# Kernel tuning notes

Hardware: AMD Instinct MI355X
Metric: run time of the kernel (lower is better)

## Reference

```python
import math
import jax, jax.numpy as jnp
import numpy as np

B, N, D_MODEL, H = 2, 4096, 2048, 16
HEAD_DIM = D_MODEL // H
CHUNK = 128  # chunk length for the lightning-attention recurrence


def _slopes(n_heads):
    # ALiBi-style slopes used by lightning attention (n_heads is a power of 2)
    start = 2.0 ** (-(2.0 ** -(math.log2(n_heads) - 3)))
    return np.array([start ** (i + 1) for i in range(n_heads)], dtype=np.float32)


def setup_inputs() -> dict:
    key = jax.random.key(0)
    kx, k1, k2, k3, k4 = jax.random.split(key, 5)
    scale = 1.0 / math.sqrt(D_MODEL)
    x = jax.random.normal(kx, (B, N, D_MODEL), dtype=jnp.float32)
    w_qkv = jax.random.normal(k1, (3 * D_MODEL, D_MODEL), dtype=jnp.float32) * scale
    b_qkv = jax.random.normal(k2, (3 * D_MODEL,), dtype=jnp.float32) * 0.01
    w_out = jax.random.normal(k3, (D_MODEL, D_MODEL), dtype=jnp.float32) * scale
    b_out = jax.random.normal(k4, (D_MODEL,), dtype=jnp.float32) * 0.01
    return {"x": x, "w_qkv": w_qkv, "b_qkv": b_qkv, "w_out": w_out, "b_out": b_out}


def _lightning_attn(q, k, v):
    # q,k,v: (B, H, N, d). Causal linear attention with per-head decay lam:
    #   S_t = lam * S_{t-1} + k_t v_t^T ;  o_t = q_t S_t
    b, h, n, d = q.shape
    nc = n // CHUNK
    lam = jnp.exp(-jnp.asarray(_slopes(h)))  # (H,)

    pos = jnp.arange(CHUNK, dtype=jnp.float32)
    decay_q = lam[:, None] ** (pos + 1.0)            # (H, C) inter-chunk q scaling
    decay_k = lam[:, None] ** (CHUNK - 1.0 - pos)    # (H, C) state-update k scaling
    diff = pos[:, None] - pos[None, :]
    causal = diff >= 0
    dmask = jnp.where(causal, lam[:, None, None] ** jnp.maximum(diff, 0.0), 0.0)  # (H,C,C)
    lam_c = lam ** CHUNK                              # (H,)

    def to_chunks(t):
        return t.reshape(b, h, nc, CHUNK, d).transpose(2, 0, 1, 3, 4)  # (nc,B,H,C,d)

    qc, kc, vc = to_chunks(q), to_chunks(k), to_chunks(v)

    def step(S, inp):
        qb, kb, vb = inp  # each (B,H,C,d); S: (B,H,d,d)
        inter = jnp.einsum('bhcd,bhde->bhce', qb * decay_q[None, :, :, None], S)
        scores = jnp.einsum('bhcd,bhed->bhce', qb, kb) * dmask[None]
        intra = jnp.einsum('bhce,bhed->bhcd', scores, vb)
        S_new = lam_c[None, :, None, None] * S + jnp.einsum(
            'bhcd,bhce->bhde', kb * decay_k[None, :, :, None], vb)
        return S_new, inter + intra

    S0 = jnp.zeros((b, h, d, d), dtype=q.dtype)
    _, out = jax.lax.scan(step, S0, (qc, kc, vc))  # out: (nc,B,H,C,d)
    return out.transpose(1, 2, 0, 3, 4).reshape(b, h, n, d)


def reference(x, w_qkv, b_qkv, w_out, b_out):
    b, n, dm = x.shape
    qkv = x @ w_qkv.T + b_qkv                         # (B,N,3D)
    q, k, v = jnp.split(qkv, 3, axis=-1)
    def heads(t):
        return t.reshape(b, n, H, HEAD_DIM).transpose(0, 2, 1, 3)  # (B,H,N,d)
    attn = _lightning_attn(heads(q), heads(k), heads(v))
    attn = attn.transpose(0, 2, 1, 3).reshape(b, n, dm)
    return attn @ w_out.T + b_out
```

## Files before the change

kernel.cpp:

```cpp
#include <hip/hip_runtime.h>
#include <stdint.h>

#define DM    2048
#define NSEQ  4096
#define BB    2
#define NH    16
#define HD    128
#define CHK   128
#define NCHK  32
#define NBH   (BB*NH)
#define MTOT  (BB*NSEQ)
#define N3    (3*DM)

typedef unsigned short u16;
typedef unsigned int   u32;
typedef __attribute__((ext_vector_type(8))) short s16x8;
typedef __attribute__((ext_vector_type(4))) short s16x4;
typedef __attribute__((ext_vector_type(4))) float f32x4;
typedef __attribute__((ext_vector_type(2))) unsigned short u16x2;

__device__ __forceinline__ float b2f(u16 b){ u32 u = ((u32)b) << 16; float f; __builtin_memcpy(&f,&u,4); return f; }
__device__ __forceinline__ u16 f2b(float f){ u32 u; __builtin_memcpy(&u,&f,4); u += 0x7fffu + ((u>>16)&1u); return (u16)(u>>16); }

__device__ __forceinline__ void gload16(const u16* g, u16* l){
  __builtin_amdgcn_global_load_lds((const __attribute__((address_space(1))) void*)g,
                                   (__attribute__((address_space(3))) void*)l, 16, 0, 0);
}

__global__ __launch_bounds__(256) void conv_bf16(const float* __restrict__ src,
                                                 u16* __restrict__ dst, int n4)
{
  for (int i = blockIdx.x*blockDim.x + threadIdx.x; i < n4; i += gridDim.x*blockDim.x){
    f32x4 v = *(const f32x4*)(src + (size_t)i*4);
    s16x4 o;
    #pragma unroll
    for (int j=0;j<4;j++) o[j] = (short)f2b(v[j]);
    *(s16x4*)(dst + (size_t)i*4) = o;
  }
}


#define GEMM256_CORE(GA_, GB_)                                                  \
  __shared__ u16 lds[65536];                                       \
  const int tid  = threadIdx.x;                                                 \
  const int lane = tid & 63;                                                    \
  const int w    = tid >> 6;                                                    \
  const int wm_i = w >> 2, wn_i = w & 3;                                        \
  const int m0 = blockIdx.y << 8;                                               \
  const int n0 = blockIdx.x << 8;                                               \
  const int l15 = lane & 15, lg = lane >> 4, l7 = lane & 7;                     \
  const int c0 = ((lg)     ^ l7) << 3;                      \
  const int c1 = ((4 + lg) ^ l7) << 3;                      \
  const int abase = wm_i*8192 + l15*64;                                         \
  const int bbase = 32768 + (wn_i>>1)*8192 + (wn_i&1)*4096 + l15*64;            \
  const int grow = lane >> 3;                                                   \
  const int gcol = ((lane & 7) ^ grow) * 8;                                     \
  const u16* gAl = GA_ + (size_t)(m0 + grow)*DM + gcol;                         \
  const u16* gBl = GB_ + (size_t)(n0 + grow)*DM + gcol;                         \
  auto STG = [&](const u16* gl, int ldsbase, int h, int kt){                    \
    _Pragma("unroll")                                                           \
    for (int j=0;j<2;j++)                                                       \
      gload16(gl + ((size_t)(h*128 + j*64 + w*8))*DM + (size_t)kt*64,           \
              lds + ldsbase + (j*64 + w*8)*64);                                 \
  };                                                                            \
  f32x4 acc[8][4];                                                              \
  _Pragma("unroll")                                                             \
  for (int m=0;m<8;m++)                                                         \
    _Pragma("unroll")                                                           \
    for (int n=0;n<4;n++) acc[m][n] = f32x4{0.f,0.f,0.f,0.f};                   \
  s16x8 bfr[4][2];                                                              \
   \
  STG(gBl, 32768,             0, 0); STG(gBl, 32768+8192,       1, 0);          \
  STG(gAl, 0,                 0, 0); STG(gAl, 8192,             1, 0);          \
  STG(gBl, 32768+16384,       0, 1); STG(gBl, 32768+16384+8192, 1, 1);          \
  asm volatile("s_waitcnt vmcnt(4)" ::: "memory");                              \
  __builtin_amdgcn_s_barrier();                                                 \
  for (int it=0; it<15; ++it){                                                  \
    const int k1 = 2*it+1, k2 = 2*it+2, k3 = 2*it+3;                            \
    PH(0,0, STG(gAl, 16384,             0, k1), );                              \
    PH(0,1, STG(gAl, 16384+8192,        1, k1), );                              \
    PH(0,2, STG(gBl, 32768,             0, k2), );                              \
    PH(0,3, STG(gBl, 32768+8192,        1, k2),                                 \
            asm volatile("s_waitcnt vmcnt(4)" ::: "memory"));                   \
    PH(1,0, STG(gAl, 0,                 0, k2), );                              \
    PH(1,1, STG(gAl, 8192,              1, k2), );                              \
    PH(1,2, STG(gBl, 32768+16384,       0, k3), );                              \
    PH(1,3, STG(gBl, 32768+16384+8192,  1, k3),                                 \
            asm volatile("s_waitcnt vmcnt(4)" ::: "memory"));                   \
  }                                                                             \
                      \
  PH(0,0, STG(gAl, 16384,      0, 31), );                                       \
  PH(0,1, STG(gAl, 16384+8192, 1, 31), );                                       \
  PH(0,2, (void)0, );                                                           \
  PH(0,3, (void)0, asm volatile("s_waitcnt vmcnt(0)" ::: "memory"));            \
  PH(1,0, (void)0, ); PH(1,1, (void)0, );                                       \
  PH(1,2, (void)0, ); PH(1,3, (void)0, );

#define PH(D, Q, STAGE, VM) do{                                                 \
  s16x8 af[2][2];                                                               \
  if ((Q)==0){                                                                  \
    _Pragma("unroll")                                                           \
    for (int n=0;n<4;n++){                                                      \
      bfr[n][0] = *(const s16x8*)(lds + bbase + (D)*16384 + n*1024 + c0);       \
      bfr[n][1] = *(const s16x8*)(lds + bbase + (D)*16384 + n*1024 + c1);       \
    }                                                                           \
  }                                                                             \
  af[0][0] = *(const s16x8*)(lds + abase + (D)*16384 + (2*(Q)  )*1024 + c0);    \
  af[0][1] = *(const s16x8*)(lds + abase + (D)*16384 + (2*(Q)  )*1024 + c1);    \
  af[1][0] = *(const s16x8*)(lds + abase + (D)*16384 + (2*(Q)+1)*1024 + c0);    \
  af[1][1] = *(const s16x8*)(lds + abase + (D)*16384 + (2*(Q)+1)*1024 + c1);    \
  STAGE;                                                                        \
  VM;                                                                           \
  __builtin_amdgcn_s_barrier();                                                 \
  __builtin_amdgcn_s_setprio(1);                                                \
  _Pragma("unroll")                                                             \
  for (int kk=0;kk<2;kk++)                                                      \
    _Pragma("unroll")                                                           \
    for (int mm=0;mm<2;mm++)                                                    \
      _Pragma("unroll")                                                         \
      for (int n=0;n<4;n++)                                                     \
        acc[2*(Q)+mm][n] = __builtin_amdgcn_mfma_f32_16x16x32_bf16(             \
            af[mm][kk], bfr[n][kk], acc[2*(Q)+mm][n], 0,0,0);                   \
  __builtin_amdgcn_s_setprio(0);                                                \
}while(0)

__global__ __launch_bounds__(512, 2) void gemm_qkv(const u16* __restrict__ Xb,
    const u16* __restrict__ Wb, const float* __restrict__ bias,
    u16* __restrict__ Qb, u16* __restrict__ Kb, u16* __restrict__ Vb)
{
  GEMM256_CORE(Xb, Wb)

  #pragma unroll
  for (int n=0;n<4;n++){
    const int gn = n0 + wn_i*64 + n*16 + l15;
    const float bv = bias[gn];
    const int which = gn >> 11;
    const int h = (gn >> 7) & 15;
    const int e = gn & 127;
    u16* base_ = (which==0) ? Qb : ((which==1) ? Kb : Vb);
    #pragma unroll
    for (int m=0;m<8;m++){
      #pragma unroll
      for (int r=0;r<4;r++){
        const int gm = m0 + wm_i*128 + m*16 + lg*4 + r;
        const int b  = gm >> 12;
        const int tt = gm & (NSEQ-1);
        base_[(((size_t)(b*NH + h))*NSEQ + tt)*HD + e] = f2b(acc[m][n][r] + bv);
      }
    }
  }
}

__global__ __launch_bounds__(512, 2) void gemm_out(const u16* __restrict__ Ab,
    const u16* __restrict__ Wb, const float* __restrict__ bias,
    float* __restrict__ Out)
{
  GEMM256_CORE(Ab, Wb)

  #pragma unroll
  for (int n=0;n<4;n++){
    const int gn = n0 + wn_i*64 + n*16 + l15;
    const float bv = bias[gn];
    #pragma unroll
    for (int m=0;m<8;m++){
      #pragma unroll
      for (int r=0;r<4;r++){
        const int gm = m0 + wm_i*128 + m*16 + lg*4 + r;
        Out[(size_t)gm*DM + gn] = acc[m][n][r] + bv;
      }
    }
  }
}

__global__ __launch_bounds__(256) void chunk_kv(const u16* __restrict__ Kb,
    const u16* __restrict__ Vb, u16* __restrict__ USb)
{
  __shared__ short Kt[128][152];
  __shared__ short Vt[128][152];
  const int tid = threadIdx.x;
  const int blk = blockIdx.x;
  const int c  = blk & (NCHK-1);
  const int bh = blk >> 5;
  const int h  = bh & (NH-1);
  const float slope = exp2f(-0.5f*(float)(h+1));

  const u16* kg = Kb + ((size_t)bh*NSEQ + (size_t)c*CHK)*HD;
  const u16* vg = Vb + ((size_t)bh*NSEQ + (size_t)c*CHK)*HD;

  const int e0 = (tid & 63) * 2;
  const int tq = tid >> 6;
  #pragma unroll
  for (int it=0; it<4; it++){
    const int tb = it*32 + tq*8;
    s16x8 k0v, k1v, v0v, v1v;
    #pragma unroll
    for (int j=0;j<8;j++){
      const int t = tb + j;
      u16x2 kv = *(const u16x2*)(kg + (size_t)t*HD + e0);
      u16x2 vv = *(const u16x2*)(vg + (size_t)t*HD + e0);
      const float dk = expf(-slope*(float)(CHK-1-t));
      k0v[j] = (short)f2b(b2f(kv[0])*dk);
      k1v[j] = (short)f2b(b2f(kv[1])*dk);
      v0v[j] = (short)vv[0];
      v1v[j] = (short)vv[1];
    }
    *(s16x8*)&Kt[e0  ][tb] = k0v;
    *(s16x8*)&Kt[e0+1][tb] = k1v;
    *(s16x8*)&Vt[e0  ][tb] = v0v;
    *(s16x8*)&Vt[e0+1][tb] = v1v;
  }
  __syncthreads();

  const int lane = tid & 63;
  const int l15 = lane & 15, lg = lane >> 4;
  const int w = tid >> 6;
  const int wm = (w >> 1) << 6, wn = (w & 1) << 6;
  f32x4 acc[4][4];
  #pragma unroll
  for (int i=0;i<4;i++)
    #pragma unroll
    for (int j=0;j<4;j++) acc[i][j] = f32x4{0.f,0.f,0.f,0.f};

  #pragma unroll
  for (int ks=0; ks<4; ks++){
    const int kk = ks*32 + lg*8;
    s16x8 af[4], bf[4];
    #pragma unroll
    for (int m=0;m<4;m++) af[m] = *(const s16x8*)&Kt[wm + m*16 + l15][kk];
    #pragma unroll
    for (int n=0;n<4;n++) bf[n] = *(const s16x8*)&Vt[wn + n*16 + l15][kk];
    #pragma unroll
    for (int m=0;m<4;m++)
      #pragma unroll
      for (int n=0;n<4;n++)
        acc[m][n] = __builtin_amdgcn_mfma_f32_16x16x32_bf16(af[m], bf[n], acc[m][n], 0,0,0);
  }

  u16* up = USb + (size_t)blk*(HD*HD);
  #pragma unroll
  for (int m=0;m<4;m++)
    #pragma unroll
    for (int n=0;n<4;n++)
      #pragma unroll
      for (int r=0;r<4;r++){
        const int d = wm + m*16 + lg*4 + r;
        const int f = wn + n*16 + l15;
        up[d*HD + f] = f2b(acc[m][n][r]);
      }
}

__global__ __launch_bounds__(256) void scan_state(u16* __restrict__ USb)
{
  const int bh = blockIdx.x >> 3;
  const int rs = blockIdx.x & 7;
  const int tid = threadIdx.x;
  const int h = bh & (NH-1);
  const float slope = exp2f(-0.5f*(float)(h+1));
  const float lamC = expf(-slope*(float)CHK);
  float s[8];
  #pragma unroll
  for (int i=0;i<8;i++) s[i]=0.f;
  u16* base = USb + (size_t)bh*NCHK*HD*HD + rs*2048;
  const int off = tid*8;
  for (int c=0;c<NCHK;c++){
    u16* p = base + (size_t)c*HD*HD + off;
    s16x8 u = *(const s16x8*)p;
    s16x8 wv;
    #pragma unroll
    for (int j=0;j<8;j++) wv[j] = (short)f2b(s[j]);
    *(s16x8*)p = wv;
    #pragma unroll
    for (int j=0;j<8;j++) s[j] = lamC*s[j] + b2f((u16)u[j]);
  }
}

__global__ __launch_bounds__(512) void attn_chunk(
    const u16* __restrict__ Qb, const u16* __restrict__ Kb, const u16* __restrict__ Vb,
    const u16* __restrict__ Sb, u16* __restrict__ ATT)
{
  __shared__ short alds[73728];
  short* Qs = alds;
  short* Ks = alds + 17408;
  short* Vt = alds + 34816;
  short* St = alds + 54272;

  const int tid = threadIdx.x;
  const int blk = blockIdx.x;
  const int c  = blk & (NCHK-1);
  const int bh = blk >> 5;
  const int b  = bh >> 4, h = bh & 15;
  const float slope = exp2f(-0.5f*(float)(h+1));

  const size_t qoff = ((size_t)bh*NSEQ + (size_t)c*CHK)*HD;

  #pragma unroll
  for (int i=0;i<4;i++){
    const int lin = i*4096 + tid*8;
    const int r = lin >> 7, e = lin & 127;
    *(s16x8*)&Qs[r*136 + e] = *(const s16x8*)(Qb + qoff + lin);
    *(s16x8*)&Ks[r*136 + e] = *(const s16x8*)(Kb + qoff + lin);
  }
  {
    const int f0 = (tid & 63)*2;
    const int tq = tid >> 6;
    const u16* vg = Vb + qoff;
    const u16* sg = Sb + ((size_t)bh*NCHK + c)*HD*HD;
    #pragma unroll
    for (int it=0; it<2; it++){
      const int t0 = it*64 + tq*8;
      s16x8 v0v, v1v, s0v, s1v;
      #pragma unroll
      for (int j=0;j<8;j++){
        u16x2 v2 = *(const u16x2*)(vg + (size_t)(t0+j)*HD + f0);
        u16x2 s2 = *(const u16x2*)(sg + (size_t)(t0+j)*HD + f0);
        v0v[j]=(short)v2[0]; v1v[j]=(short)v2[1];
        s0v[j]=(short)s2[0]; s1v[j]=(short)s2[1];
      }
      *(s16x8*)&Vt[(f0  )*152 + t0] = v0v;
      *(s16x8*)&Vt[(f0+1)*152 + t0] = v1v;
      *(s16x8*)&St[(f0  )*152 + t0] = s0v;
      *(s16x8*)&St[(f0+1)*152 + t0] = s1v;
    }
  }
  __syncthreads();

  const int lane = tid & 63;
  const int l15 = lane & 15, lg = lane >> 4;
  const int w = tid >> 6;
  const int wrow = (w >> 1) << 5;
  const int wcol = (w & 1) << 6;

  f32x4 accs[2][4], acco[2][4];
  #pragma unroll
  for (int m=0;m<2;m++)
    #pragma unroll
    for (int n=0;n<4;n++){ accs[m][n]=f32x4{0.f,0.f,0.f,0.f}; acco[m][n]=f32x4{0.f,0.f,0.f,0.f}; }

  #pragma unroll
  for (int ks=0; ks<4; ks++){
    const int kk = ks*32 + lg*8;
    s16x8 qa[2], kb_[4], sb_[4];
    #pragma unroll
    for (int m=0;m<2;m++) qa[m] = *(const s16x8*)&Qs[(wrow + m*16 + l15)*136 + kk];
    #pragma unroll
    for (int n=0;n<4;n++){
      kb_[n] = *(const s16x8*)&Ks[(wcol + n*16 + l15)*136 + kk];
      sb_[n] = *(const s16x8*)&St[(wcol + n*16 + l15)*152 + kk];
    }
    #pragma unroll
    for (int m=0;m<2;m++)
      #pragma unroll
      for (int n=0;n<4;n++){
        accs[m][n] = __builtin_amdgcn_mfma_f32_16x16x32_bf16(qa[m], kb_[n], accs[m][n], 0,0,0);
        acco[m][n] = __builtin_amdgcn_mfma_f32_16x16x32_bf16(qa[m], sb_[n], acco[m][n], 0,0,0);
      }
  }
  __syncthreads();

  #pragma unroll
  for (int m=0;m<2;m++){
    #pragma unroll
    for (int r=0;r<4;r++){
      const int t = wrow + m*16 + lg*4 + r;
      const float dq = expf(-slope*(float)(t+1));
      #pragma unroll
      for (int n=0;n<4;n++){
        const int s = wcol + n*16 + l15;
        float v = accs[m][n][r];
        v = (t >= s) ? v*expf(-slope*(float)(t-s)) : 0.f;
        Ks[t*136 + s] = (short)f2b(v);
        acco[m][n][r] *= dq;
      }
    }
  }
  __syncthreads();

  #pragma unroll
  for (int ks=0; ks<4; ks++){
    const int kk = ks*32 + lg*8;
    s16x8 sa[2], vb_[4];
    #pragma unroll
    for (int m=0;m<2;m++) sa[m] = *(const s16x8*)&Ks[(wrow + m*16 + l15)*136 + kk];
    #pragma unroll
    for (int n=0;n<4;n++) vb_[n] = *(const s16x8*)&Vt[(wcol + n*16 + l15)*152 + kk];
    #pragma unroll
    for (int m=0;m<2;m++)
      #pragma unroll
      for (int n=0;n<4;n++)
        acco[m][n] = __builtin_amdgcn_mfma_f32_16x16x32_bf16(sa[m], vb_[n], acco[m][n], 0,0,0);
  }

  u16* op = ATT + ((size_t)(b*NSEQ + c*CHK))*DM + h*HD;
  #pragma unroll
  for (int m=0;m<2;m++)
    #pragma unroll
    for (int n=0;n<4;n++)
      #pragma unroll
      for (int r=0;r<4;r++){
        const int t = wrow + m*16 + lg*4 + r;
        const int f = wcol + n*16 + l15;
        op[(size_t)t*DM + f] = f2b(acco[m][n][r]);
      }
}

extern "C" void kernel_launch(void* const* d_in, const int* in_sizes, int n_in,
                              void* d_out, int out_size, void* d_ws, size_t ws_size,
                              hipStream_t stream)
{
  const float* x     = (const float*)d_in[0];
  const float* w_qkv = (const float*)d_in[1];
  const float* b_qkv = (const float*)d_in[2];
  const float* w_out = (const float*)d_in[3];
  const float* b_out = (const float*)d_in[4];
  float* out = (float*)d_out;

  char* ws = (char*)d_ws;
  const size_t SZ = (size_t)MTOT * DM * sizeof(u16);
  u16* Qb    = (u16*)(ws);
  u16* Kb    = (u16*)(ws + SZ);
  u16* Vb    = (u16*)(ws + 2*SZ);
  u16* USb   = (u16*)(ws + 3*SZ);
  u16* ATT   = (u16*)(ws + 4*SZ);
  u16* Xb    = ATT;
  u16* Wqkvb = USb;
  u16* Woutb = Kb;

  conv_bf16 <<<dim3(2048), 256, 0, stream>>>(x,     Xb,    MTOT*DM/4);
  conv_bf16 <<<dim3(2048), 256, 0, stream>>>(w_qkv, Wqkvb, N3*DM/4);
  gemm_qkv  <<<dim3(N3/256,  MTOT/256), 512, 0, stream>>>(Xb, Wqkvb, b_qkv, Qb, Kb, Vb);
  chunk_kv  <<<dim3(NBH*NCHK),          256, 0, stream>>>(Kb, Vb, USb);
  scan_state<<<dim3(NBH*8),             256, 0, stream>>>(USb);
  attn_chunk<<<dim3(NBH*NCHK),          512, 0, stream>>>(Qb, Kb, Vb, USb, ATT);
  conv_bf16 <<<dim3(1024), 256, 0, stream>>>(w_out, Woutb, DM*DM/4);
  gemm_out  <<<dim3(DM/256,  MTOT/256), 512, 0, stream>>>(ATT, Woutb, b_out, out);
}
```

Measured before the change: 365.7 us.

## Split GEMM phases by k-half and precompute decay tables in LDS

Reorganizes the GEMM inner phase so each phase loads one k-half of the B fragments and four A fragments, issuing 16 MFMAs per phase instead of splitting by M rows. B fragment loads are spread across two phases rather than being concentrated in the first. Separately, the per-element expf decay factors in the state-chunk and attention-chunk kernels are replaced with lookups into small shared-memory tables computed once per block. The table approach adds an LDS read per element and an extra barrier in one kernel, in exchange for dropping the transcendental calls.

```diff
diff --git a/kernel.cpp b/kernel.cpp
--- a/kernel.cpp
+++ b/kernel.cpp
@@ -49,7 +49,7 @@
   const int m0 = blockIdx.y << 8;                                               \
   const int n0 = blockIdx.x << 8;                                               \
   const int l15 = lane & 15, lg = lane >> 4, l7 = lane & 7;                     \
-  const int c0 = ((lg)     ^ l7) << 3;                      \
+  const int c0 = ((lg)     ^ l7) << 3;          \
   const int c1 = ((4 + lg) ^ l7) << 3;                      \
   const int abase = wm_i*8192 + l15*64;                                         \
   const int bbase = 32768 + (wn_i>>1)*8192 + (wn_i&1)*4096 + l15*64;            \
@@ -69,7 +69,7 @@
     _Pragma("unroll")                                                           \
     for (int n=0;n<4;n++) acc[m][n] = f32x4{0.f,0.f,0.f,0.f};                   \
   s16x8 bfr[4][2];                                                              \
-   \
+           \
   STG(gBl, 32768,             0, 0); STG(gBl, 32768+8192,       1, 0);          \
   STG(gAl, 0,                 0, 0); STG(gAl, 8192,             1, 0);          \
   STG(gBl, 32768+16384,       0, 1); STG(gBl, 32768+16384+8192, 1, 1);          \
@@ -77,50 +77,46 @@
   __builtin_amdgcn_s_barrier();                                                 \
   for (int it=0; it<15; ++it){                                                  \
     const int k1 = 2*it+1, k2 = 2*it+2, k3 = 2*it+3;                            \
-    PH(0,0, STG(gAl, 16384,             0, k1), );                              \
-    PH(0,1, STG(gAl, 16384+8192,        1, k1), );                              \
-    PH(0,2, STG(gBl, 32768,             0, k2), );                              \
-    PH(0,3, STG(gBl, 32768+8192,        1, k2),                                 \
+    PH(0,0,0,1, STG(gAl, 16384,             0, k1), (void)0);                   \
+    PH(0,1,0,1, STG(gAl, 16384+8192,        1, k1), (void)0);                   \
+    PH(0,0,4,0, STG(gBl, 32768,             0, k2), (void)0);                   \
+    PH(0,1,4,0, STG(gBl, 32768+8192,        1, k2),                             \
             asm volatile("s_waitcnt vmcnt(4)" ::: "memory"));                   \
-    PH(1,0, STG(gAl, 0,                 0, k2), );                              \
-    PH(1,1, STG(gAl, 8192,              1, k2), );                              \
-    PH(1,2, STG(gBl, 32768+16384,       0, k3), );                              \
-    PH(1,3, STG(gBl, 32768+16384+8192,  1, k3),                                 \
+    PH(1,0,0,1, STG(gAl, 0,                 0, k2), (void)0);                   \
+    PH(1,1,0,1, STG(gAl, 8192,              1, k2), (void)0);                   \
+    PH(1,0,4,0, STG(gBl, 32768+16384,       0, k3), (void)0);                   \
+    PH(1,1,4,0, STG(gBl, 32768+16384+8192,  1, k3),                             \
             asm volatile("s_waitcnt vmcnt(4)" ::: "memory"));                   \
   }                                                                             \
                       \
-  PH(0,0, STG(gAl, 16384,      0, 31), );                                       \
-  PH(0,1, STG(gAl, 16384+8192, 1, 31), );                                       \
-  PH(0,2, (void)0, );                                                           \
-  PH(0,3, (void)0, asm volatile("s_waitcnt vmcnt(0)" ::: "memory"));            \
-  PH(1,0, (void)0, ); PH(1,1, (void)0, );                                       \
-  PH(1,2, (void)0, ); PH(1,3, (void)0, );
-
-#define PH(D, Q, STAGE, VM) do{                                                 \
-  s16x8 af[2][2];                                                               \
-  if ((Q)==0){                                                                  \
+  PH(0,0,0,1, STG(gAl, 16384,      0, 31), (void)0);                            \
+  PH(0,1,0,1, STG(gAl, 16384+8192, 1, 31), (void)0);                            \
+  PH(0,0,4,0, (void)0, (void)0);                                                \
+  PH(0,1,4,0, (void)0, asm volatile("s_waitcnt vmcnt(0)" ::: "memory"));        \
+  PH(1,0,0,1, (void)0, (void)0); PH(1,1,0,1, (void)0, (void)0);                 \
+  PH(1,0,4,0, (void)0, (void)0); PH(1,1,4,0, (void)0, (void)0);
+
+#define PH(D, KK, MB, BFRD, STAGE, VM) do{                                      \
+  s16x8 af[4];                                                                  \
+  const int cc_ = (KK) ? c1 : c0;                                               \
+  if (BFRD){                                                                    \
     _Pragma("unroll")                                                           \
-    for (int n=0;n<4;n++){                                                      \
-      bfr[n][0] = *(const s16x8*)(lds + bbase + (D)*16384 + n*1024 + c0);       \
-      bfr[n][1] = *(const s16x8*)(lds + bbase + (D)*16384 + n*1024 + c1);       \
-    }                                                                           \
+    for (int n=0;n<4;n++)                                                       \
+      bfr[n][KK] = *(const s16x8*)(lds + bbase + (D)*16384 + n*1024 + cc_);     \
   }                                                                             \
-  af[0][0] = *(const s16x8*)(lds + abase + (D)*16384 + (2*(Q)  )*1024 + c0);    \
-  af[0][1] = *(const s16x8*)(lds + abase + (D)*16384 + (2*(Q)  )*1024 + c1);    \
-  af[1][0] = *(const s16x8*)(lds + abase + (D)*16384 + (2*(Q)+1)*1024 + c0);    \
-  af[1][1] = *(const s16x8*)(lds + abase + (D)*16384 + (2*(Q)+1)*1024 + c1);    \
+  _Pragma("unroll")                                                             \
+  for (int j=0;j<4;j++)                                                         \
+    af[j] = *(const s16x8*)(lds + abase + (D)*16384 + ((MB)+j)*1024 + cc_);     \
   STAGE;                                                                        \
   VM;                                                                           \
   __builtin_amdgcn_s_barrier();                                                 \
   __builtin_amdgcn_s_setprio(1);                                                \
   _Pragma("unroll")                                                             \
-  for (int kk=0;kk<2;kk++)                                                      \
+  for (int j=0;j<4;j++)                                                         \
     _Pragma("unroll")                                                           \
-    for (int mm=0;mm<2;mm++)                                                    \
-      _Pragma("unroll")                                                         \
-      for (int n=0;n<4;n++)                                                     \
-        acc[2*(Q)+mm][n] = __builtin_amdgcn_mfma_f32_16x16x32_bf16(             \
-            af[mm][kk], bfr[n][kk], acc[2*(Q)+mm][n], 0,0,0);                   \
+    for (int n=0;n<4;n++)                                                       \
+      acc[(MB)+j][n] = __builtin_amdgcn_mfma_f32_16x16x32_bf16(                 \
+          af[j], bfr[n][KK], acc[(MB)+j][n], 0,0,0);                            \
   __builtin_amdgcn_s_setprio(0);                                                \
 }while(0)
 
@@ -177,6 +173,7 @@
 {
   __shared__ short Kt[128][152];
   __shared__ short Vt[128][152];
+  __shared__ float dkt[128];
   const int tid = threadIdx.x;
   const int blk = blockIdx.x;
   const int c  = blk & (NCHK-1);
@@ -184,6 +181,9 @@
   const int h  = bh & (NH-1);
   const float slope = exp2f(-0.5f*(float)(h+1));
 
+  if (tid < 128) dkt[tid] = expf(-slope*(float)(CHK-1-tid));
+  __syncthreads();
+
   const u16* kg = Kb + ((size_t)bh*NSEQ + (size_t)c*CHK)*HD;
   const u16* vg = Vb + ((size_t)bh*NSEQ + (size_t)c*CHK)*HD;
 
@@ -198,7 +198,7 @@
       const int t = tb + j;
       u16x2 kv = *(const u16x2*)(kg + (size_t)t*HD + e0);
       u16x2 vv = *(const u16x2*)(vg + (size_t)t*HD + e0);
-      const float dk = expf(-slope*(float)(CHK-1-t));
+      const float dk = dkt[t];
       k0v[j] = (short)f2b(b2f(kv[0])*dk);
       k1v[j] = (short)f2b(b2f(kv[1])*dk);
       v0v[j] = (short)vv[0];
@@ -279,6 +279,7 @@
     const u16* __restrict__ Sb, u16* __restrict__ ATT)
 {
   __shared__ short alds[73728];
+  __shared__ float qtab[132];
   short* Qs = alds;
   short* Ks = alds + 17408;
   short* Vt = alds + 34816;
@@ -291,6 +292,8 @@
   const int b  = bh >> 4, h = bh & 15;
   const float slope = exp2f(-0.5f*(float)(h+1));
 
+  if (tid < 129) qtab[tid] = expf(-slope*(float)tid);
+
   const size_t qoff = ((size_t)bh*NSEQ + (size_t)c*CHK)*HD;
 
   #pragma unroll
@@ -362,12 +365,12 @@
     #pragma unroll
     for (int r=0;r<4;r++){
       const int t = wrow + m*16 + lg*4 + r;
-      const float dq = expf(-slope*(float)(t+1));
+      const float dq = qtab[t+1];
       #pragma unroll
       for (int n=0;n<4;n++){
         const int s = wcol + n*16 + l15;
         float v = accs[m][n][r];
-        v = (t >= s) ? v*expf(-slope*(float)(t-s)) : 0.f;
+        v = (t >= s) ? v*qtab[t-s] : 0.f;
         Ks[t*136 + s] = (short)f2b(v);
         acco[m][n][r] *= dq;
       }
```

After: 361.0 us. No clear change (-1.3%).
